# Kernel tuning notes

Measured on AMD Instinct MI355X. Metric: run time of the kernel, lower is better.

Reference implementation:

```python
import jax, jax.numpy as jnp
import numpy as np

DIM = 768
NUM_HEADS = 12
HEAD_DIM = DIM // NUM_HEADS
SCALE = HEAD_DIM ** (-0.5)
WH, WW = 14, 14
NUM_EXTRA = 1
NUM_REL_DIST = (2 * WH - 1) * (2 * WW - 1) + NUM_EXTRA * (NUM_EXTRA + 2)  # 732
N_TOK = WH * WW + NUM_EXTRA  # 197
BATCH = 64


def make_rel_pos_index():
    # mirrors the torch buffer construction (meshgrid 'ij')
    coords = np.stack(np.meshgrid(np.arange(WH), np.arange(WW), indexing='ij'))  # [2,Wh,Ww]
    coords_flat = coords.reshape(2, -1)  # [2, Wh*Ww]
    rel = coords_flat[:, :, None] - coords_flat[:, None, :]  # [2, M, M]
    rel = rel.transpose(1, 2, 0).astype(np.int64)  # [M, M, 2]
    rel[:, :, 0] += WH - 1
    rel[:, :, 1] += WW - 1
    rel[:, :, 0] *= 2 * WW - 1
    idx = np.zeros((N_TOK, N_TOK), dtype=np.int64)
    idx[NUM_EXTRA:, NUM_EXTRA:] = rel.sum(-1)
    idx[0, 0:] = NUM_REL_DIST - 3
    idx[0:, 0] = NUM_REL_DIST - 2
    idx[0, 0] = NUM_REL_DIST - 1
    return jnp.asarray(idx, dtype=jnp.int32)


def setup_inputs() -> dict:
    key = jax.random.key(0)
    ks = jax.random.split(key, 7)
    x = jax.random.normal(ks[0], (BATCH, N_TOK, DIM), dtype=jnp.float32)
    qkv_w = jax.random.normal(ks[1], (3 * DIM, DIM), dtype=jnp.float32) * (DIM ** -0.5)
    q_bias = jax.random.normal(ks[2], (DIM,), dtype=jnp.float32) * 0.02
    v_bias = jax.random.normal(ks[3], (DIM,), dtype=jnp.float32) * 0.02
    rpb_table = jax.random.normal(ks[4], (NUM_REL_DIST, NUM_HEADS), dtype=jnp.float32) * 0.02
    proj_w = jax.random.normal(ks[5], (DIM, DIM), dtype=jnp.float32) * (DIM ** -0.5)
    proj_b = jax.random.normal(ks[6], (DIM,), dtype=jnp.float32) * 0.02
    rel_index = make_rel_pos_index()
    return {"x": x, "qkv_w": qkv_w, "q_bias": q_bias, "v_bias": v_bias,
            "rpb_table": rpb_table, "proj_w": proj_w, "proj_b": proj_b,
            "rel_index": rel_index}


def reference(x, qkv_w, q_bias, v_bias, rpb_table, proj_w, proj_b, rel_index):
    B, N, C = x.shape
    # qkv bias: [q_bias, zeros, v_bias]
    qkv_bias = jnp.concatenate([q_bias, jnp.zeros_like(v_bias), v_bias]).astype(x.dtype)
    qkv = x @ qkv_w.T + qkv_bias  # [B,N,3C]
    qkv = qkv.reshape(B, N, 3, NUM_HEADS, HEAD_DIM).transpose(2, 0, 3, 1, 4)  # [3,B,H,N,d]
    q, k, v = qkv[0] * SCALE, qkv[1], qkv[2]
    # fp32 scores, as in the original
    attn = jnp.einsum('bhnd,bhmd->bhnm', q.astype(jnp.float32), k.astype(jnp.float32))
    # relative position bias gather: [N,N,H] -> [H,N,N]
    bias = rpb_table[rel_index.reshape(-1)].reshape(N, N, NUM_HEADS).transpose(2, 0, 1)
    attn = jax.nn.softmax(attn + bias[None].astype(jnp.float32), axis=-1)
    out = jnp.einsum('bhnm,bhmd->bhnd', attn, v.astype(attn.dtype))
    out = out.transpose(0, 2, 1, 3).reshape(B, N, -1).astype(x.dtype)
    return out @ proj_w.T + proj_b
```

## Files before the change

### kernel.cpp

```cpp
#include <hip/hip_runtime.h>
#include <hip/hip_bf16.h>

#define DIM 768
#define NHEADS 12
#define HD 64
#define NTOK 197
#define BATCH 64
#define NTOKENS (BATCH*NTOK)
#define NPAIR (NTOK*NTOK)
#define QK_SCALE 0.125f
#define CDIM 2304

typedef short bf16x8 __attribute__((ext_vector_type(8)));
typedef float f32x4 __attribute__((ext_vector_type(4)));

#define MFMA(a,b,c) __builtin_amdgcn_mfma_f32_16x16x32_bf16(a,b,c,0,0,0)

__device__ __forceinline__ unsigned short f2bf(float f) {
    union { float f; unsigned u; } v; v.f = f;
    unsigned r = v.u + 0x7FFFu + ((v.u >> 16) & 1u);
    return (unsigned short)(r >> 16);
}

__device__ __forceinline__ float bf2f(unsigned short u) {
    union { unsigned v; float f; } x; x.v = ((unsigned)u) << 16; return x.f;
}

__device__ __forceinline__ void gload16(const unsigned short* g, unsigned short* l) {
    __builtin_amdgcn_global_load_lds(
        (const __attribute__((address_space(1))) void*)g,
        (__attribute__((address_space(3))) void*)l, 16, 0, 0);
}

__device__ __forceinline__ int xcd_swz(int orig, int nwg) {
    int q = nwg >> 3, r = nwg & 7;
    int xcd = orig & 7, idx = orig >> 3;
    return (xcd < r ? xcd * (q + 1) : r * (q + 1) + (xcd - r) * q) + idx;
}

#define NB_X 4728
#define NB_WQ 864
#define NB_WP 288
#define NB_BIAS 1820

__device__ __forceinline__ void cvt8(const float* __restrict__ s,
                                     unsigned short* __restrict__ d, int t, int n8) {
    if (t >= n8) return;
    float4 a = ((const float4*)s)[t * 2], b = ((const float4*)s)[t * 2 + 1];
    union { unsigned short u[8]; bf16x8 v; } p;
    p.u[0] = f2bf(a.x); p.u[1] = f2bf(a.y); p.u[2] = f2bf(a.z); p.u[3] = f2bf(a.w);
    p.u[4] = f2bf(b.x); p.u[5] = f2bf(b.y); p.u[6] = f2bf(b.z); p.u[7] = f2bf(b.w);
    ((bf16x8*)d)[t] = p.v;
}

__global__ __launch_bounds__(256) void prep(
    const float* __restrict__ x, const float* __restrict__ qw,
    const float* __restrict__ pw, const float* __restrict__ rpb,
    const int* __restrict__ rel,
    unsigned short* __restrict__ Xb, unsigned short* __restrict__ Wqb,
    unsigned short* __restrict__ Wpb, unsigned short* __restrict__ biasm)
{
    int bid = blockIdx.x;
    if (bid < NB_X) {
        cvt8(x, Xb, bid * 256 + threadIdx.x, NB_X * 256);
    } else if (bid < NB_X + NB_WQ) {
        cvt8(qw, Wqb, (bid - NB_X) * 256 + threadIdx.x, NB_WQ * 256);
    } else if (bid < NB_X + NB_WQ + NB_WP) {
        cvt8(pw, Wpb, (bid - NB_X - NB_WQ) * 256 + threadIdx.x, NB_WP * 256);
    } else {
        int t = (bid - NB_X - NB_WQ - NB_WP) * 256 + threadIdx.x;
        if (t < NHEADS * NPAIR) {
            int h = t / NPAIR, p = t - h * NPAIR;
            biasm[t] = f2bf(rpb[rel[p] * NHEADS + h]);
        }
    }
}

#define NKT 12
#define TMAX 6
#define BUFE 16384

#define LDA(bo, mh) do { _Pragma("unroll") for (int mi = 0; mi < 4; ++mi) { \
    af[mi][0] = *(const bf16x8*)&AsF[(bo) + abase0 + ((mh)*4+mi)*1024 + sl0*8]; \
    af[mi][1] = *(const bf16x8*)&AsF[(bo) + abase0 + ((mh)*4+mi)*1024 + sl1*8]; } } while(0)
#define LDB(bo, nh) do { _Pragma("unroll") for (int ni = 0; ni < 2; ++ni) { \
    bw[ni][0] = *(const bf16x8*)&BsF[(bo) + bbase0 + ((nh)*2+ni)*1024 + sl0*8]; \
    bw[ni][1] = *(const bf16x8*)&BsF[(bo) + bbase0 + ((nh)*2+ni)*1024 + sl1*8]; } } while(0)
#define MM(mh, nh) do { __builtin_amdgcn_s_setprio(1); \
    _Pragma("unroll") for (int mi = 0; mi < 4; ++mi) \
    _Pragma("unroll") for (int ni = 0; ni < 2; ++ni) { \
        acc[(mh)*4+mi][(nh)*2+ni] = MFMA(af[mi][0], bw[ni][0], acc[(mh)*4+mi][(nh)*2+ni]); \
        acc[(mh)*4+mi][(nh)*2+ni] = MFMA(af[mi][1], bw[ni][1], acc[(mh)*4+mi][(nh)*2+ni]); } \
    __builtin_amdgcn_s_setprio(0); } while(0)
#define SA(Ap, buf, h, kt) do { \
    gload16(Ap + asrc[2*(h)] + (kt)*64, &AsF[(buf)*BUFE + adoff[2*(h)]]); \
    gload16(Ap + asrc[2*(h)+1] + (kt)*64, &AsF[(buf)*BUFE + adoff[2*(h)+1]]); } while(0)
#define SB(Bp, buf, h, kt) do { \
    gload16(Bp + bsrc[2*(h)] + (kt)*64, &BsF[(buf)*BUFE + adoff[2*(h)]]); \
    gload16(Bp + bsrc[2*(h)+1] + (kt)*64, &BsF[(buf)*BUFE + adoff[2*(h)+1]]); } while(0)
#define BAR __builtin_amdgcn_s_barrier()
#define WVM0 asm volatile("s_waitcnt vmcnt(0)" ::: "memory")

#define KLOOP(Ap, Bp) \
    SA(Ap, 0, 0, 0); SA(Ap, 0, 1, 0); SB(Bp, 0, 0, 0); SB(Bp, 0, 1, 0); \
    WVM0; BAR; \
    for (int t = 0; t < TMAX; ++t) { \
        int k1 = 2 * t + 1, k2 = 2 * t + 2; \
        bool st = (t < TMAX - 1); \
        LDA(0, 0); LDB(0, 0); SA(Ap, 1, 0, k1);            BAR; MM(0, 0); BAR; \
        LDB(0, 1);            SA(Ap, 1, 1, k1);            BAR; MM(0, 1); BAR; \
        LDA(0, 1);            SB(Bp, 1, 0, k1);            BAR; MM(1, 1); BAR; \
        LDB(0, 0);            SB(Bp, 1, 1, k1);            BAR; MM(1, 0); WVM0; BAR; \
        LDA(BUFE, 0); LDB(BUFE, 0); if (st) SA(Ap, 0, 0, k2); BAR; MM(0, 0); BAR; \
        LDB(BUFE, 1);               if (st) SA(Ap, 0, 1, k2); BAR; MM(0, 1); BAR; \
        LDA(BUFE, 1);               if (st) SB(Bp, 0, 0, k2); BAR; MM(1, 1); BAR; \
        LDB(BUFE, 0);               if (st) SB(Bp, 0, 1, k2); BAR; MM(1, 0); \
        if (st) { WVM0; } BAR; \
    }

__global__ __launch_bounds__(512, 2) void gemm_qkv8(
    const unsigned short* __restrict__ Xb, const unsigned short* __restrict__ Wb,
    const float* __restrict__ qbias, const float* __restrict__ vbias,
    unsigned short* __restrict__ QKVb)
{
    __shared__ __attribute__((aligned(16))) unsigned short AsF[2 * BUFE];
    __shared__ __attribute__((aligned(16))) unsigned short BsF[2 * BUFE];
    int tid = threadIdx.x, lane = tid & 63, wid = tid >> 6;
    int wr = wid >> 2, wc = wid & 3;
    int wg = xcd_swz(blockIdx.x, 450);
    int bx = wg / 9, by = wg % 9;
    int m0 = bx * 256, n0 = by * 256;
    int r15 = lane & 15, hi = lane >> 4, sx = lane & 7;
    int sl0 = hi ^ sx, sl1 = (hi + 4) ^ sx;

    size_t asrc[4], bsrc[4];
    int adoff[4];
    #pragma unroll
    for (int i = 0; i < 4; ++i) {
        int c = i * 512 + tid;
        int row = c >> 3, s = c & 7, rr = row & 127, half = row >> 7;
        int slot = s ^ (rr & 7);
        int ar = m0 + row; if (ar >= NTOKENS) ar = NTOKENS - 1;
        asrc[i] = (size_t)ar * DIM + slot * 8;
        bsrc[i] = (size_t)(n0 + row) * DIM + slot * 8;
        adoff[i] = half * 8192 + rr * 64 + s * 8;
    }
    int abase0 = wr * 8192 + r15 * 64;
    int bbase0 = (wc >> 1) * 8192 + (wc & 1) * 4096 + r15 * 64;

    f32x4 acc[8][4];
    #pragma unroll
    for (int i = 0; i < 8; ++i)
        #pragma unroll
        for (int j = 0; j < 4; ++j) acc[i][j] = (f32x4){0.f, 0.f, 0.f, 0.f};

    bf16x8 af[4][2], bw[2][2];
    KLOOP(Xb, Wb)

    unsigned short* reg = (wid < 4) ? &AsF[wid * 8192] : &BsF[(wid - 4) * 8192];
    {
        int which = n0 / DIM;
        float scl = (which == 0) ? QK_SCALE : 1.f;
        #pragma unroll
        for (int n = 0; n < 4; ++n) {
            int colr = n0 - which * DIM + wc * 64 + n * 16 + r15;
            float bv = (which == 0) ? qbias[colr] : (which == 2 ? vbias[colr] : 0.f);
            #pragma unroll
            for (int m = 0; m < 8; ++m) {
                int lrb = m * 16 + hi * 4;
                #pragma unroll
                for (int r = 0; r < 4; ++r) {
                    int lr = lrb + r;
                    int c = n * 16 + r15;
                    reg[lr * 64 + (c ^ (((lr >> 2) & 3) << 4))] =
                        f2bf((acc[m][n][r] + bv) * scl);
                }
            }
        }
    }
    #pragma unroll
    for (int it = 0; it < 16; ++it) {
        int c = it * 64 + lane;
        int lr = c >> 3, cc = c & 7;
        int row = m0 + wr * 128 + lr;
        if (row < NTOKENS) {
            bf16x8 v = *(bf16x8*)&reg[lr * 64 + ((cc * 8) ^ (((lr >> 2) & 3) << 4))];
            *(bf16x8*)(QKVb + (size_t)row * CDIM + n0 + wc * 64 + cc * 8) = v;
        }
    }
}

__global__ __launch_bounds__(256, 2) void gemm_proj(
    const unsigned short* __restrict__ Ob, const unsigned short* __restrict__ Wp,
    const float* __restrict__ pbias, float* __restrict__ out)
{
    __shared__ __attribute__((aligned(16))) unsigned short As[128 * 64];
    __shared__ __attribute__((aligned(16))) unsigned short Bs[128 * 64];
    int tid = threadIdx.x, lane = tid & 63, wid = tid >> 6;
    int wg = xcd_swz(blockIdx.x, 594);
    int bx = wg / 6, by = wg % 6;
    int m0 = bx * 128, n0 = by * 128;
    int wm = (wid >> 1) * 64, wn = (wid & 1) * 64;

    size_t abase[4], bbase[4];
    unsigned short *alds[4], *blds[4];
    #pragma unroll
    for (int i = 0; i < 4; ++i) {
        int chunk = i * 4 + wid;
        int row = chunk * 8 + (lane >> 3);
        int slot = (lane & 7) ^ (row & 7);
        int ar = m0 + row; if (ar >= NTOKENS) ar = NTOKENS - 1;
        abase[i] = (size_t)ar * DIM + slot * 8;
        bbase[i] = (size_t)(n0 + row) * DIM + slot * 8;
        alds[i] = &As[chunk * 512];
        blds[i] = &Bs[chunk * 512];
    }
    int r15 = lane & 15, hi = lane >> 4, sx = lane & 7;
    int s0 = (hi ^ sx) * 8, s1 = ((hi + 4) ^ sx) * 8;
    int arow[4], brow[4];
    #pragma unroll
    for (int i = 0; i < 4; ++i) {
        arow[i] = (wm + i * 16 + r15) * 64;
        brow[i] = (wn + i * 16 + r15) * 64;
    }

    f32x4 acc[4][4];
    #pragma unroll
    for (int i = 0; i < 4; ++i)
        #pragma unroll
        for (int j = 0; j < 4; ++j) acc[i][j] = (f32x4){0.f, 0.f, 0.f, 0.f};

    for (int k0 = 0; k0 < DIM; k0 += 64) {
        __syncthreads();
        #pragma unroll
        for (int i = 0; i < 4; ++i) {
            gload16(Ob + abase[i] + k0, alds[i]);
            gload16(Wp + bbase[i] + k0, blds[i]);
        }
        __syncthreads();
        #pragma unroll
        for (int ks = 0; ks < 2; ++ks) {
            int so = ks ? s1 : s0;
            bf16x8 af[4], bwv[4];
            #pragma unroll
            for (int i = 0; i < 4; ++i) af[i] = *(bf16x8*)&As[arow[i] + so];
            #pragma unroll
            for (int j = 0; j < 4; ++j) bwv[j] = *(bf16x8*)&Bs[brow[j] + so];
            __builtin_amdgcn_s_setprio(1);
            #pragma unroll
            for (int i = 0; i < 4; ++i)
                #pragma unroll
                for (int j = 0; j < 4; ++j)
                    acc[i][j] = MFMA(af[i], bwv[j], acc[i][j]);
            __builtin_amdgcn_s_setprio(0);
        }
    }

    #pragma unroll
    for (int j = 0; j < 4; ++j) {
        int col = n0 + wn + j * 16 + r15;
        float bv = pbias[col];
        #pragma unroll
        for (int i = 0; i < 4; ++i) {
            #pragma unroll
            for (int r = 0; r < 4; ++r) {
                int row = m0 + wm + i * 16 + hi * 4 + r;
                if (row < NTOKENS)
                    out[(size_t)row * DIM + col] = acc[i][j][r] + bv;
            }
        }
    }
}

#define KP 72
#define PP 232
#define VPITCH 256

__global__ __launch_bounds__(256, 2) void attn(
    const unsigned short* __restrict__ QKV, const unsigned short* __restrict__ biasm,
    unsigned short* __restrict__ O)
{
    __shared__ __attribute__((aligned(16))) unsigned short VT[64 * VPITCH];
    __shared__ __attribute__((aligned(16))) unsigned short KlPl[208 * KP];

    int tid = threadIdx.x, lane = tid & 63, wid = tid >> 6;
    int r15 = lane & 15, hi = lane >> 4;
    int wg = blockIdx.x;
    int g = wg >> 5, qt = (wg >> 3) & 3, p = wg & 7;
    int bh = g * 8 + p;
    int h = bh % NHEADS, b = bh / NHEADS;
    size_t tb = (size_t)b * NTOK;
    int hq = h * 64;
    int rbase = qt * 64 + wid * 16 + hi * 4;

    int kcol = (tid & 7) * 8;
    bf16x8 kreg[7];
    #pragma unroll
    for (int t = 0; t < 7; ++t) {
        int row = t * 32 + (tid >> 3);
        int rc = row < NTOK ? row : (NTOK - 1);
        kreg[t] = *(const bf16x8*)(QKV + (tb + rc) * CDIM + 768 + hq + kcol);
    }
    #pragma unroll
    for (int t = 0; t < 7; ++t) {
        int row = t * 32 + (tid >> 3);
        if (row < NTOK)
            *(bf16x8*)&KlPl[row * KP + kcol] = kreg[t];
    }

    bf16x8 v0r[4], v1r[4];
    #pragma unroll
    for (int it = 0; it < 4; ++it) {
        int c = it * 256 + tid;
        int rp = c >> 3, kc = c & 7;
        int r0 = 2 * rp, r1 = 2 * rp + 1;
        bf16x8 z = (bf16x8)(short)0;
        v0r[it] = z; v1r[it] = z;
        if (r0 < NTOK) v0r[it] = *(const bf16x8*)(QKV + (tb + r0) * CDIM + 1536 + hq + kc * 8);
        if (r1 < NTOK) v1r[it] = *(const bf16x8*)(QKV + (tb + r1) * CDIM + 1536 + hq + kc * 8);
    }

    int qrow_g = qt * 64 + wid * 16 + r15;
    int qsrc = qrow_g < NTOK ? qrow_g : (NTOK - 1);
    bf16x8 aq[2];
    #pragma unroll
    for (int ks = 0; ks < 2; ++ks)
        aq[ks] = *(const bf16x8*)(QKV + (tb + qsrc) * CDIM + hq + ks * 32 + hi * 8);

    unsigned short breg[4][13];
    {
        const unsigned short* bb = biasm + h * NPAIR;
        #pragma unroll
        for (int r = 0; r < 4; ++r) {
            int row_g = rbase + r;
            int rowc = row_g < NTOK ? row_g : (NTOK - 1);
            const unsigned short* brow = bb + rowc * NTOK + r15;
            #pragma unroll
            for (int t = 0; t < 13; ++t) {
                int off = t * 16;
                if (t == 12 && r15 >= 5) off = 0;
                breg[r][t] = brow[off];
            }
        }
    }
    __syncthreads();

    f32x4 sa[13];
    #pragma unroll
    for (int t = 0; t < 13; ++t) sa[t] = (f32x4){0.f,0.f,0.f,0.f};
    __builtin_amdgcn_s_setprio(1);
    #pragma unroll
    for (int t = 0; t < 13; ++t) {
        #pragma unroll
        for (int ks = 0; ks < 2; ++ks) {
            bf16x8 bk = *(bf16x8*)&KlPl[(t * 16 + r15) * KP + ks * 32 + hi * 8];
            sa[t] = MFMA(aq[ks], bk, sa[t]);
        }
    }
    __builtin_amdgcn_s_setprio(0);
    __syncthreads();

    #pragma unroll
    for (int it = 0; it < 4; ++it) {
        int c = it * 256 + tid;
        int rp = c >> 3, kc = c & 7;
        if (rp < 112) {
            #pragma unroll
            for (int j = 0; j < 8; ++j) {
                unsigned int w = (unsigned int)(unsigned short)v0r[it][j] |
                                 ((unsigned int)(unsigned short)v1r[it][j] << 16);
                int slot2 = (rp >> 2) ^ j ^ kc;
                *(unsigned int*)&VT[(kc * 8 + j) * VPITCH + slot2 * 8 + (rp & 3) * 2] = w;
            }
        }
    }

    int plbase = wid * (16 * PP);
    float invr[4];
    #pragma unroll
    for (int r = 0; r < 4; ++r) {
        #pragma unroll
        for (int t = 0; t < 13; ++t) {
            int col = t * 16 + r15;
            if (col < NTOK) sa[t][r] += bf2f(breg[r][t]);
            else            sa[t][r] = -1e30f;
        }
        float mx = sa[0][r];
        #pragma unroll
        for (int t = 1; t < 13; ++t) mx = fmaxf(mx, sa[t][r]);
        #pragma unroll
        for (int m = 1; m < 16; m <<= 1) mx = fmaxf(mx, __shfl_xor(mx, m));
        float sum = 0.f;
        #pragma unroll
        for (int t = 0; t < 13; ++t) {
            float e = __expf(sa[t][r] - mx);
            sa[t][r] = e; sum += e;
        }
        int roff = plbase + (hi * 4 + r) * PP;
        #pragma unroll
        for (int t = 0; t < 13; ++t)
            KlPl[roff + t * 16 + r15] = f2bf(sa[t][r]);
        KlPl[roff + 208 + r15] = 0;
        #pragma unroll
        for (int m = 1; m < 16; m <<= 1) sum += __shfl_xor(sum, m);
        invr[r] = __builtin_amdgcn_rcpf(sum);
    }
    __syncthreads();

    f32x4 oa[4];
    #pragma unroll
    for (int dt = 0; dt < 4; ++dt) oa[dt] = (f32x4){0.f,0.f,0.f,0.f};
    int X = hi ^ (r15 & 7) ^ (r15 >> 3);
    __builtin_amdgcn_s_setprio(1);
    #pragma unroll
    for (int ks = 0; ks < 7; ++ks) {
        bf16x8 ap = *(bf16x8*)&KlPl[plbase + r15 * PP + ks * 32 + hi * 8];
        #pragma unroll
        for (int dt = 0; dt < 4; ++dt) {
            int d = dt * 16 + r15;
            int slotp = (ks * 4) ^ (dt * 2) ^ X;
            bf16x8 bv = *(bf16x8*)&VT[d * VPITCH + slotp * 8];
            oa[dt] = MFMA(ap, bv, oa[dt]);
        }
    }
    __builtin_amdgcn_s_setprio(0);

    #pragma unroll
    for (int dt = 0; dt < 4; ++dt)
        #pragma unroll
        for (int r = 0; r < 4; ++r)
            KlPl[plbase + (hi * 4 + r) * 72 + dt * 16 + r15] = f2bf(oa[dt][r] * invr[r]);
    #pragma unroll
    for (int it = 0; it < 2; ++it) {
        int c = it * 64 + lane;
        int lr = c >> 3, cc = c & 7;
        int qrow = qt * 64 + wid * 16 + lr;
        if (qrow < NTOK)
            *(bf16x8*)(O + (tb + qrow) * DIM + hq + cc * 8) =
                *(bf16x8*)&KlPl[plbase + lr * 72 + cc * 8];
    }
}

extern "C" void kernel_launch(void* const* d_in, const int* in_sizes, int n_in,
                              void* d_out, int out_size, void* d_ws, size_t ws_size,
                              hipStream_t stream) {
    const float* x      = (const float*)d_in[0];
    const float* qkv_w  = (const float*)d_in[1];
    const float* q_bias = (const float*)d_in[2];
    const float* v_bias = (const float*)d_in[3];
    const float* rpb    = (const float*)d_in[4];
    const float* proj_w = (const float*)d_in[5];
    const float* proj_b = (const float*)d_in[6];
    const int*   rel    = (const int*)d_in[7];
    float* out = (float*)d_out;

    const size_t NELEM = (size_t)NTOKENS * DIM;
    const size_t WQKV  = (size_t)3 * DIM * DIM;
    const size_t WPROJ = (size_t)DIM * DIM;
    unsigned short* Xb   = (unsigned short*)d_ws;
    unsigned short* Wqb  = Xb + NELEM;
    unsigned short* Wpb  = Wqb + WQKV;
    unsigned short* QKVb = Wpb + WPROJ;
    unsigned short* biasm = QKVb + (size_t)NTOKENS * CDIM;
    unsigned short* Ob = Xb;

    prep<<<NB_X + NB_WQ + NB_WP + NB_BIAS, 256, 0, stream>>>(
        x, qkv_w, proj_w, rpb, rel, Xb, Wqb, Wpb, biasm);

    gemm_qkv8<<<450, 512, 0, stream>>>(Xb, Wqb, q_bias, v_bias, QKVb);

    attn<<<3072, 256, 0, stream>>>(QKVb, biasm, Ob);

    gemm_proj<<<594, 256, 0, stream>>>(Ob, Wpb, proj_b, out);
}
```

Baseline: 151.4 us.

## Replace 256x256 pipelined QKV GEMM with simpler 128x128 single-buffer kernel

Swaps the 512-thread, 256x256-tile, double-buffered, barrier-interleaved QKV GEMM for a 256-thread 128x128-tile kernel modeled on the projection GEMM, using one LDS buffer and a plain load/sync/compute loop. With 1782 blocks instead of 450, the grid fills the CUs better and tail waves are smaller. The cost is lower operand reuse per tile, more global traffic, and no overlap of loads with MFMA.

After: 155.0 us. 1.02x slower.

```diff
diff --git a/kernel.cpp b/kernel.cpp
--- a/kernel.cpp
+++ b/kernel.cpp
@@ -76,116 +76,102 @@
     }
 }
 
-#define NKT 12
-#define TMAX 6
-#define BUFE 16384
-
-#define LDA(bo, mh) do { _Pragma("unroll") for (int mi = 0; mi < 4; ++mi) { \
-    af[mi][0] = *(const bf16x8*)&AsF[(bo) + abase0 + ((mh)*4+mi)*1024 + sl0*8]; \
-    af[mi][1] = *(const bf16x8*)&AsF[(bo) + abase0 + ((mh)*4+mi)*1024 + sl1*8]; } } while(0)
-#define LDB(bo, nh) do { _Pragma("unroll") for (int ni = 0; ni < 2; ++ni) { \
-    bw[ni][0] = *(const bf16x8*)&BsF[(bo) + bbase0 + ((nh)*2+ni)*1024 + sl0*8]; \
-    bw[ni][1] = *(const bf16x8*)&BsF[(bo) + bbase0 + ((nh)*2+ni)*1024 + sl1*8]; } } while(0)
-#define MM(mh, nh) do { __builtin_amdgcn_s_setprio(1); \
-    _Pragma("unroll") for (int mi = 0; mi < 4; ++mi) \
-    _Pragma("unroll") for (int ni = 0; ni < 2; ++ni) { \
-        acc[(mh)*4+mi][(nh)*2+ni] = MFMA(af[mi][0], bw[ni][0], acc[(mh)*4+mi][(nh)*2+ni]); \
-        acc[(mh)*4+mi][(nh)*2+ni] = MFMA(af[mi][1], bw[ni][1], acc[(mh)*4+mi][(nh)*2+ni]); } \
-    __builtin_amdgcn_s_setprio(0); } while(0)
-#define SA(Ap, buf, h, kt) do { \
-    gload16(Ap + asrc[2*(h)] + (kt)*64, &AsF[(buf)*BUFE + adoff[2*(h)]]); \
-    gload16(Ap + asrc[2*(h)+1] + (kt)*64, &AsF[(buf)*BUFE + adoff[2*(h)+1]]); } while(0)
-#define SB(Bp, buf, h, kt) do { \
-    gload16(Bp + bsrc[2*(h)] + (kt)*64, &BsF[(buf)*BUFE + adoff[2*(h)]]); \
-    gload16(Bp + bsrc[2*(h)+1] + (kt)*64, &BsF[(buf)*BUFE + adoff[2*(h)+1]]); } while(0)
-#define BAR __builtin_amdgcn_s_barrier()
-#define WVM0 asm volatile("s_waitcnt vmcnt(0)" ::: "memory")
-
-#define KLOOP(Ap, Bp) \
-    SA(Ap, 0, 0, 0); SA(Ap, 0, 1, 0); SB(Bp, 0, 0, 0); SB(Bp, 0, 1, 0); \
-    WVM0; BAR; \
-    for (int t = 0; t < TMAX; ++t) { \
-        int k1 = 2 * t + 1, k2 = 2 * t + 2; \
-        bool st = (t < TMAX - 1); \
-        LDA(0, 0); LDB(0, 0); SA(Ap, 1, 0, k1);            BAR; MM(0, 0); BAR; \
-        LDB(0, 1);            SA(Ap, 1, 1, k1);            BAR; MM(0, 1); BAR; \
-        LDA(0, 1);            SB(Bp, 1, 0, k1);            BAR; MM(1, 1); BAR; \
-        LDB(0, 0);            SB(Bp, 1, 1, k1);            BAR; MM(1, 0); WVM0; BAR; \
-        LDA(BUFE, 0); LDB(BUFE, 0); if (st) SA(Ap, 0, 0, k2); BAR; MM(0, 0); BAR; \
-        LDB(BUFE, 1);               if (st) SA(Ap, 0, 1, k2); BAR; MM(0, 1); BAR; \
-        LDA(BUFE, 1);               if (st) SB(Bp, 0, 0, k2); BAR; MM(1, 1); BAR; \
-        LDB(BUFE, 0);               if (st) SB(Bp, 0, 1, k2); BAR; MM(1, 0); \
-        if (st) { WVM0; } BAR; \
-    }
-
-__global__ __launch_bounds__(512, 2) void gemm_qkv8(
+__global__ __launch_bounds__(256, 2) void gemm_qkv128(
     const unsigned short* __restrict__ Xb, const unsigned short* __restrict__ Wb,
     const float* __restrict__ qbias, const float* __restrict__ vbias,
     unsigned short* __restrict__ QKVb)
 {
-    __shared__ __attribute__((aligned(16))) unsigned short AsF[2 * BUFE];
-    __shared__ __attribute__((aligned(16))) unsigned short BsF[2 * BUFE];
+    __shared__ __attribute__((aligned(16))) unsigned short As[128 * 64];
+    __shared__ __attribute__((aligned(16))) unsigned short Bs[128 * 64];
     int tid = threadIdx.x, lane = tid & 63, wid = tid >> 6;
-    int wr = wid >> 2, wc = wid & 3;
-    int wg = xcd_swz(blockIdx.x, 450);
-    int bx = wg / 9, by = wg % 9;
-    int m0 = bx * 256, n0 = by * 256;
+    int wg = xcd_swz(blockIdx.x, 1782);
+    int bx = wg / 18, by = wg % 18;
+    int m0 = bx * 128, n0 = by * 128;
+    int wm = (wid >> 1) * 64, wn = (wid & 1) * 64;
+
+    size_t abase[4], bbase[4];
+    unsigned short *alds[4], *blds[4];
+    #pragma unroll
+    for (int i = 0; i < 4; ++i) {
+        int chunk = i * 4 + wid;
+        int row = chunk * 8 + (lane >> 3);
+        int slot = (lane & 7) ^ (row & 7);
+        int ar = m0 + row; if (ar >= NTOKENS) ar = NTOKENS - 1;
+        abase[i] = (size_t)ar * DIM + slot * 8;
+        bbase[i] = (size_t)(n0 + row) * DIM + slot * 8;
+        alds[i] = &As[chunk * 512];
+        blds[i] = &Bs[chunk * 512];
+    }
     int r15 = lane & 15, hi = lane >> 4, sx = lane & 7;
-    int sl0 = hi ^ sx, sl1 = (hi + 4) ^ sx;
-
-    size_t asrc[4], bsrc[4];
-    int adoff[4];
+    int s0 = (hi ^ sx) * 8, s1 = ((hi + 4) ^ sx) * 8;
+    int arow[4], brow[4];
     #pragma unroll
     for (int i = 0; i < 4; ++i) {
-        int c = i * 512 + tid;
-        int row = c >> 3, s = c & 7, rr = row & 127, half = row >> 7;
-        int slot = s ^ (rr & 7);
-        int ar = m0 + row; if (ar >= NTOKENS) ar = NTOKENS - 1;
-        asrc[i] = (size_t)ar * DIM + slot * 8;
-        bsrc[i] = (size_t)(n0 + row) * DIM + slot * 8;
-        adoff[i] = half * 8192 + rr * 64 + s * 8;
-    }
-    int abase0 = wr * 8192 + r15 * 64;
-    int bbase0 = (wc >> 1) * 8192 + (wc & 1) * 4096 + r15 * 64;
-
-    f32x4 acc[8][4];
-    #pragma unroll
-    for (int i = 0; i < 8; ++i)
+        arow[i] = (wm + i * 16 + r15) * 64;
+        brow[i] = (wn + i * 16 + r15) * 64;
+    }
+
+    f32x4 acc[4][4];
+    #pragma unroll
+    for (int i = 0; i < 4; ++i)
         #pragma unroll
         for (int j = 0; j < 4; ++j) acc[i][j] = (f32x4){0.f, 0.f, 0.f, 0.f};
 
-    bf16x8 af[4][2], bw[2][2];
-    KLOOP(Xb, Wb)
-
-    unsigned short* reg = (wid < 4) ? &AsF[wid * 8192] : &BsF[(wid - 4) * 8192];
+    for (int k0 = 0; k0 < DIM; k0 += 64) {
+        __syncthreads();
+        #pragma unroll
+        for (int i = 0; i < 4; ++i) {
+            gload16(Xb + abase[i] + k0, alds[i]);
+            gload16(Wb + bbase[i] + k0, blds[i]);
+        }
+        __syncthreads();
+        #pragma unroll
+        for (int ks = 0; ks < 2; ++ks) {
+            int so = ks ? s1 : s0;
+            bf16x8 af[4], bwv[4];
+            #pragma unroll
+            for (int i = 0; i < 4; ++i) af[i] = *(bf16x8*)&As[arow[i] + so];
+            #pragma unroll
+            for (int j = 0; j < 4; ++j) bwv[j] = *(bf16x8*)&Bs[brow[j] + so];
+            __builtin_amdgcn_s_setprio(1);
+            #pragma unroll
+            for (int i = 0; i < 4; ++i)
+                #pragma unroll
+                for (int j = 0; j < 4; ++j)
+                    acc[i][j] = MFMA(af[i], bwv[j], acc[i][j]);
+            __builtin_amdgcn_s_setprio(0);
+        }
+    }
+    __syncthreads();
+
+    unsigned short* reg = (wid < 2) ? &As[wid * 4096] : &Bs[(wid - 2) * 4096];
     {
         int which = n0 / DIM;
         float scl = (which == 0) ? QK_SCALE : 1.f;
         #pragma unroll
-        for (int n = 0; n < 4; ++n) {
-            int colr = n0 - which * DIM + wc * 64 + n * 16 + r15;
+        for (int j = 0; j < 4; ++j) {
+            int colr = n0 - which * DIM + wn + j * 16 + r15;
             float bv = (which == 0) ? qbias[colr] : (which == 2 ? vbias[colr] : 0.f);
             #pragma unroll
-            for (int m = 0; m < 8; ++m) {
-                int lrb = m * 16 + hi * 4;
+            for (int i = 0; i < 4; ++i) {
                 #pragma unroll
                 for (int r = 0; r < 4; ++r) {
-                    int lr = lrb + r;
-                    int c = n * 16 + r15;
+                    int lr = i * 16 + hi * 4 + r;
+                    int c = j * 16 + r15;
                     reg[lr * 64 + (c ^ (((lr >> 2) & 3) << 4))] =
-                        f2bf((acc[m][n][r] + bv) * scl);
+                        f2bf((acc[i][j][r] + bv) * scl);
                 }
             }
         }
     }
     #pragma unroll
-    for (int it = 0; it < 16; ++it) {
+    for (int it = 0; it < 8; ++it) {
         int c = it * 64 + lane;
         int lr = c >> 3, cc = c & 7;
-        int row = m0 + wr * 128 + lr;
+        int row = m0 + wm + lr;
         if (row < NTOKENS) {
             bf16x8 v = *(bf16x8*)&reg[lr * 64 + ((cc * 8) ^ (((lr >> 2) & 3) << 4))];
-            *(bf16x8*)(QKVb + (size_t)row * CDIM + n0 + wc * 64 + cc * 8) = v;
+            *(bf16x8*)(QKVb + (size_t)row * CDIM + n0 + wn + cc * 8) = v;
         }
     }
 }
@@ -467,7 +453,7 @@
     prep<<<NB_X + NB_WQ + NB_WP + NB_BIAS, 256, 0, stream>>>(
         x, qkv_w, proj_w, rpb, rel, Xb, Wqb, Wpb, biasm);
 
-    gemm_qkv8<<<450, 512, 0, stream>>>(Xb, Wqb, q_bias, v_bias, QKVb);
+    gemm_qkv128<<<1782, 256, 0, stream>>>(Xb, Wqb, q_bias, v_bias, QKVb);
 
     attn<<<3072, 256, 0, stream>>>(QKVb, biasm, Ob);
 
```
